# Optimization experiments

Hardware: AMD Instinct MI355X
Metric: run time of the kernel (lower is better)

## Reference

```python
import jax, jax.numpy as jnp
import numpy as np

IN_FEATURES = 4096
OUT_FEATURES = 11008


def setup_inputs() -> dict:
    key = jax.random.key(0)
    kx, kw, ks, kb = jax.random.split(key, 4)
    x = jax.random.normal(kx, (64, IN_FEATURES), dtype=jnp.float32)
    # int8 quantized weight, stored as int32 for portability (values in [-128, 127])
    weight_quantized = jax.random.randint(kw, (OUT_FEATURES, IN_FEATURES), -128, 128, dtype=jnp.int32)
    # per-tensor scale, as produced by quantize_weights_int8: |w|.max()/127
    weight_scale = jnp.asarray(0.01, dtype=jnp.float32)
    bias = jax.random.normal(kb, (OUT_FEATURES,), dtype=jnp.float32) * 0.02
    return {"x": x, "weight_quantized": weight_quantized, "weight_scale": weight_scale, "bias": bias}


def reference(x, weight_quantized, weight_scale, bias):
    # dequantize_weights_int8: q.float() * scale, then F.linear(x, W, b) = x @ W.T + b
    weight = weight_quantized.astype(jnp.float32) * weight_scale  # [out, in]
    return jnp.einsum('mi,oi->mo', x, weight) + bias
```

## Files before the change

kernel.cpp:

```cpp
#include <hip/hip_runtime.h>
#include <hip/hip_bf16.h>


#define M_DIM 64
#define N_DIM 11008
#define K_DIM 4096
#define KSPLIT 8
#define KC (K_DIM / KSPLIT)
#define BK 128
#define LDS_STRIDE 136
#define BLOCK_N 64

typedef __attribute__((ext_vector_type(8))) short bf16x8;
typedef __attribute__((ext_vector_type(4))) float f32x4;
typedef __attribute__((ext_vector_type(4))) int i32x4;
typedef __attribute__((ext_vector_type(4))) short s16x4;

__device__ __forceinline__ short i2bf(int q) {
    float f = (float)q;
    return (short)(__builtin_bit_cast(unsigned int, f) >> 16);
}

__device__ __forceinline__ short f2bf(float f) {
    unsigned int u = __builtin_bit_cast(unsigned int, f);
    u = u + 0x7FFFu + ((u >> 16) & 1u);
    return (short)(u >> 16);
}

__global__ __launch_bounds__(256) void init_bias_kernel(const float* __restrict__ bias,
                                                        float* __restrict__ out) {
    int idx = blockIdx.x * 256 + threadIdx.x;
    int col4 = idx % 2752;
    f32x4 b = *(const f32x4*)(bias + col4 * 4);
    *(f32x4*)(out + (size_t)idx * 4) = b;
}

__global__ __launch_bounds__(256) void qlinear_kernel(const float* __restrict__ x,
                                                      const int* __restrict__ wq,
                                                      const float* __restrict__ scale_p,
                                                      float* __restrict__ out) {
    __shared__ short lds[M_DIM * LDS_STRIDE];

    const int tid  = threadIdx.x;
    const int wave = tid >> 6;
    const int lane = tid & 63;
    const int quad = lane >> 4;
    const int l16  = lane & 15;

    const int n0  = blockIdx.x * BLOCK_N;
    const int kc0 = blockIdx.y * KC;
    const float scale = *scale_p;

    const int nw = n0 + wave * 16 + l16;
    const int* wptr = wq + (size_t)nw * K_DIM + kc0 + quad * 8;

    f32x4 acc[4] = {f32x4{0,0,0,0}, f32x4{0,0,0,0}, f32x4{0,0,0,0}, f32x4{0,0,0,0}};

    for (int kb = 0; kb < KC; kb += BK) {
        {
            const float* xbase = x + kc0 + kb;
            #pragma unroll
            for (int j = 0; j < 8; ++j) {
                int f  = tid + j * 256;
                int row = f >> 5;
                int c4  = f & 31;
                f32x4 v = *(const f32x4*)(xbase + (size_t)row * K_DIM + c4 * 4);
                s16x4 h;
                h.x = f2bf(v.x); h.y = f2bf(v.y); h.z = f2bf(v.z); h.w = f2bf(v.w);
                *(s16x4*)&lds[row * LDS_STRIDE + c4 * 4] = h;
            }
        }
        __syncthreads();

        #pragma unroll
        for (int kk = 0; kk < BK; kk += 32) {
            i32x4 b0 = *(const i32x4*)(wptr + kb + kk);
            i32x4 b1 = *(const i32x4*)(wptr + kb + kk + 4);
            bf16x8 bfrag;
            bfrag[0] = i2bf(b0.x); bfrag[1] = i2bf(b0.y);
            bfrag[2] = i2bf(b0.z); bfrag[3] = i2bf(b0.w);
            bfrag[4] = i2bf(b1.x); bfrag[5] = i2bf(b1.y);
            bfrag[6] = i2bf(b1.z); bfrag[7] = i2bf(b1.w);

            #pragma unroll
            for (int mi = 0; mi < 4; ++mi) {
                bf16x8 afrag = *(const bf16x8*)&lds[(mi * 16 + l16) * LDS_STRIDE + kk + quad * 8];
                acc[mi] = __builtin_amdgcn_mfma_f32_16x16x32_bf16(afrag, bfrag, acc[mi], 0, 0, 0);
            }
        }
        __syncthreads();
    }

    const int nout = n0 + wave * 16 + l16;
    #pragma unroll
    for (int mi = 0; mi < 4; ++mi) {
        #pragma unroll
        for (int r = 0; r < 4; ++r) {
            int m = mi * 16 + quad * 4 + r;
            atomicAdd(&out[(size_t)m * N_DIM + nout], acc[mi][r] * scale);
        }
    }
}

extern "C" void kernel_launch(void* const* d_in, const int* in_sizes, int n_in,
                              void* d_out, int out_size, void* d_ws, size_t ws_size,
                              hipStream_t stream) {
    const float* x      = (const float*)d_in[0];
    const int*   wq     = (const int*)d_in[1];
    const float* scale  = (const float*)d_in[2];
    const float* bias   = (const float*)d_in[3];
    float* out = (float*)d_out;

    init_bias_kernel<<<688, 256, 0, stream>>>(bias, out);

    dim3 grid(N_DIM / BLOCK_N, KSPLIT);
    qlinear_kernel<<<grid, 256, 0, stream>>>(x, wq, scale, out);
}
```

Measured before the change: 259.8 us.

## Pre-convert x to bf16, use single-wave GEMM blocks, replace atomics with split-K reduce

x is converted to bf16 once in a separate kernel and read straight from global memory by the GEMM, which drops the per-block LDS staging and barriers. The GEMM now uses 64-thread blocks, each covering 16 output columns, with KSPLIT cut from 8 to 4. Weight loads are nontemporal. Partial sums go to a workspace and a reduce kernel applies scale and bias, replacing the bias-init kernel and the atomics. The cost is 45 MB of partial-sum traffic, one extra launch, and x being re-read through cache by every block.

```diff
diff --git a/kernel.cpp b/kernel.cpp
--- a/kernel.cpp
+++ b/kernel.cpp
@@ -5,114 +5,115 @@
 #define M_DIM 64
 #define N_DIM 11008
 #define K_DIM 4096
-#define KSPLIT 8
+#define KSPLIT 4
 #define KC (K_DIM / KSPLIT)
-#define BK 128
-#define LDS_STRIDE 136
-#define BLOCK_N 64
+#define OUT_ELEMS (M_DIM * N_DIM)
 
 typedef __attribute__((ext_vector_type(8))) short bf16x8;
 typedef __attribute__((ext_vector_type(4))) float f32x4;
 typedef __attribute__((ext_vector_type(4))) int i32x4;
-typedef __attribute__((ext_vector_type(4))) short s16x4;
-
-__device__ __forceinline__ short i2bf(int q) {
-    float f = (float)q;
-    return (short)(__builtin_bit_cast(unsigned int, f) >> 16);
-}
+typedef __attribute__((ext_vector_type(8))) short s16x8;
 
 __device__ __forceinline__ short f2bf(float f) {
     unsigned int u = __builtin_bit_cast(unsigned int, f);
     u = u + 0x7FFFu + ((u >> 16) & 1u);
     return (short)(u >> 16);
 }
-
-__global__ __launch_bounds__(256) void init_bias_kernel(const float* __restrict__ bias,
-                                                        float* __restrict__ out) {
-    int idx = blockIdx.x * 256 + threadIdx.x;
-    int col4 = idx % 2752;
-    f32x4 b = *(const f32x4*)(bias + col4 * 4);
-    *(f32x4*)(out + (size_t)idx * 4) = b;
+__device__ __forceinline__ short i2bf(int q) {
+    float f = (float)q;
+    return (short)(__builtin_bit_cast(unsigned int, f) >> 16);
 }
 
-__global__ __launch_bounds__(256) void qlinear_kernel(const float* __restrict__ x,
-                                                      const int* __restrict__ wq,
-                                                      const float* __restrict__ scale_p,
-                                                      float* __restrict__ out) {
-    __shared__ short lds[M_DIM * LDS_STRIDE];
+__global__ __launch_bounds__(256) void convert_x_kernel(const float* __restrict__ x,
+                                                        short* __restrict__ xs) {
+    int idx = blockIdx.x * 256 + threadIdx.x;
+    const f32x4* p = (const f32x4*)x + (size_t)idx * 2;
+    f32x4 a = p[0], b = p[1];
+    s16x8 h;
+    h[0] = f2bf(a.x); h[1] = f2bf(a.y); h[2] = f2bf(a.z); h[3] = f2bf(a.w);
+    h[4] = f2bf(b.x); h[5] = f2bf(b.y); h[6] = f2bf(b.z); h[7] = f2bf(b.w);
+    *((s16x8*)xs + idx) = h;
+}
 
-    const int tid  = threadIdx.x;
-    const int wave = tid >> 6;
-    const int lane = tid & 63;
+__global__ __launch_bounds__(64) void qgemm_kernel(const short* __restrict__ xs,
+                                                   const int* __restrict__ wq,
+                                                   float* __restrict__ part) {
+    const int lane = threadIdx.x;
     const int quad = lane >> 4;
     const int l16  = lane & 15;
+    const int n0   = blockIdx.x * 16;
+    const int ks   = blockIdx.y;
+    const int kc0  = ks * KC;
 
-    const int n0  = blockIdx.x * BLOCK_N;
-    const int kc0 = blockIdx.y * KC;
-    const float scale = *scale_p;
-
-    const int nw = n0 + wave * 16 + l16;
-    const int* wptr = wq + (size_t)nw * K_DIM + kc0 + quad * 8;
+    const int* wrow = wq + (size_t)(n0 + l16) * K_DIM + kc0 + quad * 8;
+    const short* xrow = xs + (size_t)l16 * K_DIM + kc0 + quad * 8;
 
     f32x4 acc[4] = {f32x4{0,0,0,0}, f32x4{0,0,0,0}, f32x4{0,0,0,0}, f32x4{0,0,0,0}};
 
-    for (int kb = 0; kb < KC; kb += BK) {
-        {
-            const float* xbase = x + kc0 + kb;
-            #pragma unroll
-            for (int j = 0; j < 8; ++j) {
-                int f  = tid + j * 256;
-                int row = f >> 5;
-                int c4  = f & 31;
-                f32x4 v = *(const f32x4*)(xbase + (size_t)row * K_DIM + c4 * 4);
-                s16x4 h;
-                h.x = f2bf(v.x); h.y = f2bf(v.y); h.z = f2bf(v.z); h.w = f2bf(v.w);
-                *(s16x4*)&lds[row * LDS_STRIDE + c4 * 4] = h;
-            }
-        }
-        __syncthreads();
+    #pragma unroll 4
+    for (int kk = 0; kk < KC; kk += 32) {
+        i32x4 b0 = __builtin_nontemporal_load((const i32x4*)(wrow + kk));
+        i32x4 b1 = __builtin_nontemporal_load((const i32x4*)(wrow + kk + 4));
+        bf16x8 bfrag;
+        bfrag[0] = i2bf(b0.x); bfrag[1] = i2bf(b0.y);
+        bfrag[2] = i2bf(b0.z); bfrag[3] = i2bf(b0.w);
+        bfrag[4] = i2bf(b1.x); bfrag[5] = i2bf(b1.y);
+        bfrag[6] = i2bf(b1.z); bfrag[7] = i2bf(b1.w);
 
         #pragma unroll
-        for (int kk = 0; kk < BK; kk += 32) {
-            i32x4 b0 = *(const i32x4*)(wptr + kb + kk);
-            i32x4 b1 = *(const i32x4*)(wptr + kb + kk + 4);
-            bf16x8 bfrag;
-            bfrag[0] = i2bf(b0.x); bfrag[1] = i2bf(b0.y);
-            bfrag[2] = i2bf(b0.z); bfrag[3] = i2bf(b0.w);
-            bfrag[4] = i2bf(b1.x); bfrag[5] = i2bf(b1.y);
-            bfrag[6] = i2bf(b1.z); bfrag[7] = i2bf(b1.w);
-
-            #pragma unroll
-            for (int mi = 0; mi < 4; ++mi) {
-                bf16x8 afrag = *(const bf16x8*)&lds[(mi * 16 + l16) * LDS_STRIDE + kk + quad * 8];
-                acc[mi] = __builtin_amdgcn_mfma_f32_16x16x32_bf16(afrag, bfrag, acc[mi], 0, 0, 0);
-            }
+        for (int mi = 0; mi < 4; ++mi) {
+            bf16x8 afrag = *(const bf16x8*)(xrow + (size_t)mi * 16 * K_DIM + kk);
+            acc[mi] = __builtin_amdgcn_mfma_f32_16x16x32_bf16(afrag, bfrag, acc[mi], 0, 0, 0);
         }
-        __syncthreads();
     }
 
-    const int nout = n0 + wave * 16 + l16;
+    float* ps = part + (size_t)ks * OUT_ELEMS + n0 + l16;
     #pragma unroll
     for (int mi = 0; mi < 4; ++mi) {
         #pragma unroll
         for (int r = 0; r < 4; ++r) {
             int m = mi * 16 + quad * 4 + r;
-            atomicAdd(&out[(size_t)m * N_DIM + nout], acc[mi][r] * scale);
+            ps[(size_t)m * N_DIM] = acc[mi][r];
         }
     }
+}
+
+__global__ __launch_bounds__(256) void reduce_kernel(const float* __restrict__ part,
+                                                     const float* __restrict__ scale_p,
+                                                     const float* __restrict__ bias,
+                                                     float* __restrict__ out) {
+    int i4 = blockIdx.x * 256 + threadIdx.x;
+    float s = *scale_p;
+    int col4 = i4 % 2752;
+    f32x4 b = *(const f32x4*)(bias + col4 * 4);
+    f32x4 a0 = *((const f32x4*)part + i4);
+    f32x4 a1 = *((const f32x4*)(part + (size_t)OUT_ELEMS) + i4);
+    f32x4 a2 = *((const f32x4*)(part + (size_t)2 * OUT_ELEMS) + i4);
+    f32x4 a3 = *((const f32x4*)(part + (size_t)3 * OUT_ELEMS) + i4);
+    f32x4 r;
+    r.x = (a0.x + a1.x + a2.x + a3.x) * s + b.x;
+    r.y = (a0.y + a1.y + a2.y + a3.y) * s + b.y;
+    r.z = (a0.z + a1.z + a2.z + a3.z) * s + b.z;
+    r.w = (a0.w + a1.w + a2.w + a3.w) * s + b.w;
+    *((f32x4*)out + i4) = r;
 }
 
 extern "C" void kernel_launch(void* const* d_in, const int* in_sizes, int n_in,
                               void* d_out, int out_size, void* d_ws, size_t ws_size,
                               hipStream_t stream) {
-    const float* x      = (const float*)d_in[0];
-    const int*   wq     = (const int*)d_in[1];
-    const float* scale  = (const float*)d_in[2];
-    const float* bias   = (const float*)d_in[3];
+    const float* x     = (const float*)d_in[0];
+    const int*   wq    = (const int*)d_in[1];
+    const float* scale = (const float*)d_in[2];
+    const float* bias  = (const float*)d_in[3];
     float* out = (float*)d_out;
 
-    init_bias_kernel<<<688, 256, 0, stream>>>(bias, out);
+    float* part = (float*)d_ws;
+    short* xs   = (short*)((char*)d_ws + (size_t)KSPLIT * OUT_ELEMS * 4);
 
-    dim3 grid(N_DIM / BLOCK_N, KSPLIT);
-    qlinear_kernel<<<grid, 256, 0, stream>>>(x, wq, scale, out);
+    convert_x_kernel<<<128, 256, 0, stream>>>(x, xs);
+
+    dim3 grid(N_DIM / 16, KSPLIT);
+    qgemm_kernel<<<grid, 64, 0, stream>>>(xs, wq, part);
+
+    reduce_kernel<<<688, 256, 0, stream>>>(part, scale, bias, out);
 }
```

Result: slower. 289.6 us (+11.5%).
